# Optimization experiments

Hardware: AMD Instinct MI355X
Metric: run time of the kernel (lower is better)

The kernel has to match this reference:

```python
import jax, jax.numpy as jnp
import numpy as np

N = 50000      # nodes
E = 400000     # edges
IN = 128       # in_channels
HID = 64       # hidden_channels (per head)
H = 4          # heads
OUT = 10       # classes
G = 64         # graphs in batch


def setup_inputs() -> dict:
    key = jax.random.key(0)
    ks = jax.random.split(key, 32)
    s = 0.05
    inp = {
        "x": jax.random.normal(ks[0], (N, IN), dtype=jnp.float32),
        "edge_index": jax.random.randint(ks[1], (2, E), 0, N, dtype=jnp.int32),
        "batch": jnp.sort(jax.random.randint(ks[2], (N,), 0, G, dtype=jnp.int32)),
    }
    # TransformerConv layer 1 params (in=IN -> heads*HID)
    d1 = H * HID
    inp["Wq1"] = jax.random.normal(ks[3], (IN, d1)) * s
    inp["bq1"] = jnp.zeros((d1,), jnp.float32)
    inp["Wk1"] = jax.random.normal(ks[4], (IN, d1)) * s
    inp["bk1"] = jnp.zeros((d1,), jnp.float32)
    inp["Wv1"] = jax.random.normal(ks[5], (IN, d1)) * s
    inp["bv1"] = jnp.zeros((d1,), jnp.float32)
    inp["Ws1"] = jax.random.normal(ks[6], (IN, d1)) * s   # root/skip weight
    inp["bs1"] = jnp.zeros((d1,), jnp.float32)
    # TransformerConv layer 2 params (in=H*HID -> heads*HID)
    inp["Wq2"] = jax.random.normal(ks[7], (d1, d1)) * s
    inp["bq2"] = jnp.zeros((d1,), jnp.float32)
    inp["Wk2"] = jax.random.normal(ks[8], (d1, d1)) * s
    inp["bk2"] = jnp.zeros((d1,), jnp.float32)
    inp["Wv2"] = jax.random.normal(ks[9], (d1, d1)) * s
    inp["bv2"] = jnp.zeros((d1,), jnp.float32)
    inp["Ws2"] = jax.random.normal(ks[10], (d1, d1)) * s
    inp["bs2"] = jnp.zeros((d1,), jnp.float32)
    # final classifier
    inp["Wl"] = jax.random.normal(ks[11], (d1, OUT)) * s
    inp["bl"] = jnp.zeros((OUT,), jnp.float32)
    return inp


def transformer_conv(x, src, dst, Wq, bq, Wk, bk, Wv, bv, Ws, bs):
    """PyG TransformerConv (concat=True, root_weight=True, beta=None, eval mode).
    src = edge_index[0] (source j), dst = edge_index[1] (target i).
    """
    n = x.shape[0]
    q = (x @ Wq + bq).reshape(n, H, HID)
    k = (x @ Wk + bk).reshape(n, H, HID)
    v = (x @ Wv + bv).reshape(n, H, HID)
    # per-edge attention logits [E, H]
    alpha = jnp.einsum('ehc,ehc->eh', q[dst], k[src]) / np.sqrt(HID).astype(np.float32)
    # scatter-softmax over incoming edges of each target node
    amax = jax.ops.segment_max(alpha, dst, num_segments=n)           # [N, H], -inf for isolated
    ex = jnp.exp(alpha - amax[dst])                                   # [E, H]
    denom = jax.ops.segment_sum(ex, dst, num_segments=n) + 1e-16      # [N, H]
    w = ex / denom[dst]                                               # normalized alpha [E, H]
    # scatter-sum aggregation of weighted values
    out = jax.ops.segment_sum(w[:, :, None] * v[src], dst, num_segments=n)  # [N, H, HID]
    out = out.reshape(n, H * HID)
    return out + (x @ Ws + bs)  # root/skip connection


def reference(x, edge_index, batch,
              Wq1, bq1, Wk1, bk1, Wv1, bv1, Ws1, bs1,
              Wq2, bq2, Wk2, bk2, Wv2, bv2, Ws2, bs2,
              Wl, bl):
    src, dst = edge_index[0], edge_index[1]
    h = jax.nn.elu(transformer_conv(x, src, dst, Wq1, bq1, Wk1, bk1, Wv1, bv1, Ws1, bs1))
    h = jax.nn.elu(transformer_conv(h, src, dst, Wq2, bq2, Wk2, bk2, Wv2, bv2, Ws2, bs2))
    # global mean pool per graph
    sums = jax.ops.segment_sum(h, batch, num_segments=G)              # [G, H*HID]
    cnt = jax.ops.segment_sum(jnp.ones((h.shape[0],), h.dtype), batch, num_segments=G)
    pooled = sums / jnp.maximum(cnt, 1.0)[:, None]
    logits = pooled @ Wl + bl
    return jax.nn.log_softmax(logits, axis=-1)
```

## Files before the change

### kernel.cpp

```cpp
#include <hip/hip_runtime.h>
#include <math.h>

constexpr int NN   = 50000;
constexpr int NE   = 400000;
constexpr int INC  = 128;
constexpr int NH   = 4;
constexpr int D1   = 256;
constexpr int D4   = 1024;
constexpr int NOUT = 10;
constexpr int NG   = 64;
constexpr int NB_SCAN = (NN + 255) / 256;


typedef __attribute__((ext_vector_type(8))) short bf16x8;
typedef __attribute__((ext_vector_type(4))) float f32x4;
typedef __attribute__((ext_vector_type(2))) float f32x2;

__device__ __forceinline__ short f2b(float f) {
  union { float f; unsigned int i; } v; v.f = f;
  unsigned int x = v.i;
  return (short)((x + 0x7FFFu + ((x >> 16) & 1u)) >> 16);
}
__device__ __forceinline__ float b2f(short u) {
  union { unsigned int i; float f; } v; v.i = ((unsigned int)(unsigned short)u) << 16;
  return v.f;
}
__device__ __forceinline__ float4 ld4b(const short* p) {
  short4 u = *(const short4*)p;
  return make_float4(b2f(u.x), b2f(u.y), b2f(u.z), b2f(u.w));
}
__device__ __forceinline__ int pk_fp8x4(float a, float b, float c, float d) {
  int v = __builtin_amdgcn_cvt_pk_fp8_f32(a, b, 0, false);
  v = __builtin_amdgcn_cvt_pk_fp8_f32(c, d, v, true);
  return v;
}

__device__ __forceinline__ void gld_lds16(const short* g, short* l) {
  __builtin_amdgcn_global_load_lds(
      (const __attribute__((address_space(1))) unsigned int*)g,
      (__attribute__((address_space(3))) unsigned int*)l, 16, 0, 0);
}

constexpr int CVT_XB  = (NN * INC / 4 + 255) / 256;
constexpr int CVT_W1B = (4 * D1 * INC + 255) / 256;
constexpr int CVT_W2B = (4 * D1 * D1 + 255) / 256;
constexpr int CVT_BB  = 8;
constexpr int CVT_DB  = (NN + 255) / 256;
constexpr int CVT_SB  = (NG * D1 + 255) / 256;

__device__ __forceinline__ void wt_one(const float* Wq, const float* Wk,
    const float* Wv, const float* Ws, short* Wt, int kbits, int i) {
  int K = 1 << kbits;
  int seg = i >> (kbits + 8);
  int idx = i & ((D1 << kbits) - 1);
  int n = idx >> kbits, k = idx & (K - 1);
  const float* W = (seg == 0) ? Wq : (seg == 1) ? Wk : (seg == 2) ? Wv : Ws;
  int row;
  if (seg == 0)      row = n;
  else if (seg == 3) row = 768 + n;
  else               row = 256 + (n >> 2) * 8 + ((seg == 2) ? 4 : 0) + (n & 3);
  Wt[(size_t)row * K + k] = f2b(W[(size_t)k * D1 + n]);
}

__global__ void cvt_all_k(const float* __restrict__ x, short* __restrict__ Xb,
    const float* __restrict__ Wq1, const float* __restrict__ Wk1,
    const float* __restrict__ Wv1, const float* __restrict__ Ws1,
    const float* __restrict__ Wq2, const float* __restrict__ Wk2,
    const float* __restrict__ Wv2, const float* __restrict__ Ws2,
    short* __restrict__ Wtc1, short* __restrict__ Wtc2,
    const float* __restrict__ bq1, const float* __restrict__ bk1,
    const float* __restrict__ bv1, const float* __restrict__ bs1,
    const float* __restrict__ bq2, const float* __restrict__ bk2,
    const float* __restrict__ bv2, const float* __restrict__ bs2,
    float* __restrict__ bc1, float* __restrict__ bc2,
    int* __restrict__ deg, float* __restrict__ sums) {
  const int b = blockIdx.x;
  const int t = threadIdx.x;
  if (b < CVT_XB) {
    int i = (b * 256 + t) * 4;
    if (i >= NN * INC) return;
    float4 v = *(const float4*)(x + i);
    short4 o; o.x = f2b(v.x); o.y = f2b(v.y); o.z = f2b(v.z); o.w = f2b(v.w);
    *(short4*)(Xb + i) = o;
  } else if (b < CVT_XB + CVT_W1B) {
    int i = (b - CVT_XB) * 256 + t;
    if (i < 4 * D1 * INC) wt_one(Wq1, Wk1, Wv1, Ws1, Wtc1, 7, i);
  } else if (b < CVT_XB + CVT_W1B + CVT_W2B) {
    int i = (b - CVT_XB - CVT_W1B) * 256 + t;
    if (i < 4 * D1 * D1) wt_one(Wq2, Wk2, Wv2, Ws2, Wtc2, 8, i);
  } else if (b < CVT_XB + CVT_W1B + CVT_W2B + CVT_BB) {
    int i = (b - CVT_XB - CVT_W1B - CVT_W2B) * 256 + t;
    if (i >= 2 * D4) return;
    int row = i & (D4 - 1);
    const float* bq = (i < D4) ? bq1 : bq2;
    const float* bk = (i < D4) ? bk1 : bk2;
    const float* bv = (i < D4) ? bv1 : bv2;
    const float* bs = (i < D4) ? bs1 : bs2;
    float v;
    if (row < 256) v = bq[row];
    else if (row < 768) {
      int j = row - 256, grp = j >> 3, off = j & 7;
      int ch = grp * 4 + (off & 3);
      v = (off < 4) ? bk[ch] : bv[ch];
    } else v = bs[row - 768];
    ((i < D4) ? bc1 : bc2)[row] = v;
  } else if (b < CVT_XB + CVT_W1B + CVT_W2B + CVT_BB + CVT_DB) {
    int i = (b - CVT_XB - CVT_W1B - CVT_W2B - CVT_BB) * 256 + t;
    if (i < NN) deg[i] = 0;
  } else {
    int i = (b - CVT_XB - CVT_W1B - CVT_W2B - CVT_BB - CVT_DB) * 256 + t;
    if (i < NG * D1) sums[i] = 0.f;
  }
}

__global__ void deg_count(const int* __restrict__ dst, int* __restrict__ deg) {
  int e = blockIdx.x * 256 + threadIdx.x;
  if (e < NE) atomicAdd(&deg[dst[e]], 1);
}
__global__ __launch_bounds__(256) void scan1(const int* __restrict__ deg,
    int* __restrict__ partial, const int* __restrict__ batch, int* __restrict__ gb) {
  if (blockIdx.x == NB_SCAN) {
    int g = threadIdx.x;
    if (g > NG) return;
    int lo = 0, hi = NN;
    while (lo < hi) {
      int mid = (lo + hi) >> 1;
      if (batch[mid] < g) lo = mid + 1; else hi = mid;
    }
    gb[g] = lo;
    return;
  }
  __shared__ int sh[256];
  int t = threadIdx.x, i = blockIdx.x * 256 + t;
  sh[t] = (i < NN) ? deg[i] : 0;
  __syncthreads();
  for (int off = 128; off > 0; off >>= 1) {
    if (t < off) sh[t] += sh[t + off];
    __syncthreads();
  }
  if (t == 0) partial[blockIdx.x] = sh[0];
}
__global__ __launch_bounds__(256) void scan3(const int* __restrict__ deg,
    const int* __restrict__ partial, int* __restrict__ rowstart,
    int* __restrict__ cursor) {
  __shared__ int sh[256];
  __shared__ int base_s;
  const int t = threadIdx.x;
  int pv = (t < NB_SCAN) ? partial[t] : 0;
  sh[t] = pv;
  __syncthreads();
  for (int off = 1; off < 256; off <<= 1) {
    int o = (t >= off) ? sh[t - off] : 0;
    __syncthreads();
    sh[t] += o;
    __syncthreads();
  }
  if (t == 0) base_s = (blockIdx.x == 0) ? 0 : sh[blockIdx.x - 1];
  __syncthreads();
  const int base = base_s;
  __syncthreads();
  int i = blockIdx.x * 256 + t;
  int v = (i < NN) ? deg[i] : 0;
  sh[t] = v;
  __syncthreads();
  for (int off = 1; off < 256; off <<= 1) {
    int o = (t >= off) ? sh[t - off] : 0;
    __syncthreads();
    sh[t] += o;
    __syncthreads();
  }
  int excl = sh[t] - v + base;
  if (i <= NN) rowstart[i] = excl;
  if (i < NN)  cursor[i]   = excl;
}
__global__ void scatter_k(const int* __restrict__ src, const int* __restrict__ dst,
    int* __restrict__ cursor, int* __restrict__ esrc) {
  int e = blockIdx.x * 256 + threadIdx.x;
  if (e >= NE) return;
  int d = dst[e];
  int pos = atomicAdd(&cursor[d], 1);
  esrc[pos] = src[e];
}

constexpr int CLDS = 136;

__global__ __launch_bounds__(256) void gemm_mfma(
    const short* __restrict__ Xb, const short* __restrict__ Wt,
    const float* __restrict__ bias, short* __restrict__ QS,
    unsigned char* __restrict__ KV8, int M, int K) {
  __shared__ short smem[128 * CLDS];
  const int bx = blockIdx.x;
  const int by = blockIdx.y;
  const int m_tile = (bx & 7) + (by << 3);
  const int n_tile = bx >> 3;
  const int m0 = m_tile * 128;
  if (m0 >= M) return;
  const int n0 = n_tile * 128;

  const int t    = threadIdx.x;
  const int lane = t & 63;
  const int wv   = t >> 6;
  const int wm   = (wv >> 1) * 64;
  const int wn   = (wv & 1) * 64;
  const int quad = lane >> 4;
  const int l16  = lane & 15;
  const int lrow = lane >> 2;
  const int lseg = lane & 3;

  const int swz_w = (lseg ^ ((lrow >> 1) & 3)) * 8;
  const int swz_r = (quad ^ ((l16 >> 1) & 3)) * 8;

  f32x4 acc[4][4] = {};

  {
#pragma unroll
    for (int j = 0; j < 2; ++j) {
      const int rb = (wv * 2 + j) * 16;
      int gm = m0 + rb + lrow;
      gm = gm < M ? gm : M - 1;
      gld_lds16(Xb + (size_t)gm * K + swz_w,              &smem[rb * 32]);
      gld_lds16(Wt + (size_t)(n0 + rb + lrow) * K + swz_w, &smem[4096 + rb * 32]);
    }
  }
  __syncthreads();

  int cur = 0;
  for (int k0 = 0; k0 < K; k0 += 32) {
    if (k0 + 32 < K) {
      short* An = &smem[(cur ^ 1) * 8192];
      short* Bn = &smem[(cur ^ 1) * 8192 + 4096];
#pragma unroll
      for (int j = 0; j < 2; ++j) {
        const int rb = (wv * 2 + j) * 16;
        int gm = m0 + rb + lrow;
        gm = gm < M ? gm : M - 1;
        gld_lds16(Xb + (size_t)gm * K + k0 + 32 + swz_w,              &An[rb * 32]);
        gld_lds16(Wt + (size_t)(n0 + rb + lrow) * K + k0 + 32 + swz_w, &Bn[rb * 32]);
      }
    }
    {
      const short* Ac = &smem[cur * 8192];
      const short* Bc = &smem[cur * 8192 + 4096];
      bf16x8 a[4], b[4];
#pragma unroll
      for (int mi = 0; mi < 4; mi++)
        a[mi] = *(const bf16x8*)(&Ac[(wm + mi * 16 + l16) * 32 + swz_r]);
#pragma unroll
      for (int nj = 0; nj < 4; nj++)
        b[nj] = *(const bf16x8*)(&Bc[(wn + nj * 16 + l16) * 32 + swz_r]);
#pragma unroll
      for (int mi = 0; mi < 4; mi++)
#pragma unroll
        for (int nj = 0; nj < 4; nj++)
          acc[mi][nj] = __builtin_amdgcn_mfma_f32_16x16x32_bf16(b[nj], a[mi], acc[mi][nj], 0, 0, 0);
    }
    __syncthreads();
    cur ^= 1;
  }

  const bool isKV = (n_tile >= 2) && (n_tile <= 5);
  float4 bz[4];
#pragma unroll
  for (int nj = 0; nj < 4; nj++)
    bz[nj] = *(const float4*)(bias + n0 + wn + nj * 16 + quad * 4);

  if (isKV) {
    unsigned char* cs = (unsigned char*)smem;
#pragma unroll
    for (int mi = 0; mi < 4; mi++) {
      const int row = wm + mi * 16 + l16;
#pragma unroll
      for (int nj = 0; nj < 4; nj++) {
        const int colb = wn + nj * 16 + quad * 4;
        const int p = pk_fp8x4(acc[mi][nj][0] + bz[nj].x, acc[mi][nj][1] + bz[nj].y,
                               acc[mi][nj][2] + bz[nj].z, acc[mi][nj][3] + bz[nj].w);
        *(int*)(cs + row * 136 + colb) = p;
      }
    }
    __syncthreads();
    const int kv_base = n0 - 256;
#pragma unroll
    for (int it = 0; it < 8; ++it) {
      const int chunk = it * 256 + t;
      const int row = chunk >> 4;
      const int cb  = (chunk & 15) * 8;
      const int gm  = m0 + row;
      if (gm >= M) continue;
      *(int2*)(KV8 + (size_t)gm * 512 + kv_base + cb) = *(const int2*)(cs + row * 136 + cb);
    }
  } else {
#pragma unroll
    for (int mi = 0; mi < 4; mi++) {
      const int row = wm + mi * 16 + l16;
#pragma unroll
      for (int nj = 0; nj < 4; nj++) {
        const int col = wn + nj * 16 + quad * 4;
        short4 o;
        o.x = f2b(acc[mi][nj][0] + bz[nj].x);
        o.y = f2b(acc[mi][nj][1] + bz[nj].y);
        o.z = f2b(acc[mi][nj][2] + bz[nj].z);
        o.w = f2b(acc[mi][nj][3] + bz[nj].w);
        *(short4*)(&smem[row * CLDS + col]) = o;
      }
    }
    __syncthreads();
    const int qs_base = (n_tile < 2) ? n0 : (n0 - 512);
#pragma unroll
    for (int it = 0; it < 8; ++it) {
      const int chunk = it * 256 + t;
      const int row = chunk >> 4;
      const int cc  = (chunk & 15) * 8;
      const int gm  = m0 + row;
      if (gm >= M) continue;
      const int4 s4 = *(const int4*)(&smem[row * CLDS + cc]);
      *(int4*)(QS + (size_t)gm * 512 + qs_base + cc) = s4;
    }
  }
}

__device__ __forceinline__ f32x2 cvt_lo(int x) { return __builtin_amdgcn_cvt_pk_f32_fp8(x, false); }
__device__ __forceinline__ f32x2 cvt_hi(int x) { return __builtin_amdgcn_cvt_pk_f32_fp8(x, true); }

template <int CTRL>
__device__ __forceinline__ float ror_add(float x) {
  int y = __builtin_amdgcn_update_dpp(0, __float_as_int(x), CTRL, 0xF, 0xF, true);
  return x + __int_as_float(y);
}
__device__ __forceinline__ float red16(float x) {
  x = ror_add<0x121>(x);
  x = ror_add<0x122>(x);
  x = ror_add<0x124>(x);
  x = ror_add<0x128>(x);
  return x;
}

#define SC2 (0.125f * 1.44269504088896341f)

__device__ __forceinline__ float edge_score(const int2 x, f32x2 q01, f32x2 q23,
                                            f32x2& vv01, f32x2& vv23) {
  f32x2 kk01 = cvt_lo(x.x), kk23 = cvt_hi(x.x);
  vv01 = cvt_lo(x.y); vv23 = cvt_hi(x.y);
  f32x2 dd = q01 * kk01;
  dd += q23 * kk23;
  return red16(dd.x + dd.y);
}

template <typename TOUT>
__device__ __forceinline__ void st1(TOUT* p, float v);
template <> __device__ __forceinline__ void st1<float>(float* p, float v) { *p = v; }
template <> __device__ __forceinline__ void st1<short>(short* p, float v) { *p = f2b(v); }

template <typename TOUT>
__global__ __launch_bounds__(256) void node_attn(
    const int* __restrict__ rowstart, const int* __restrict__ esrc,
    const short* __restrict__ QS, const unsigned char* __restrict__ KV8,
    TOUT* __restrict__ out) {
  const int nid = blockIdx.x * 4 + (threadIdx.x >> 6);
  if (nid >= NN) return;
  const int t  = threadIdx.x & 63;
  const int c0 = t * 4;
  const int r0 = __builtin_amdgcn_readfirstlane(rowstart[nid]);
  const int r1 = __builtin_amdgcn_readfirstlane(rowstart[nid + 1]);
  const short4 qu = *(const short4*)(QS + (size_t)nid * 512 + c0);
  const f32x2 q01 = {b2f(qu.x), b2f(qu.y)};
  const f32x2 q23 = {b2f(qu.z), b2f(qu.w)};
  const unsigned char* kvb = KV8 + t * 8;
  float m = -INFINITY, denom = 0.f;
  f32x2 a01 = {0.f, 0.f}, a23 = {0.f, 0.f};
  int r = r0;
  for (; r + 7 < r1; r += 8) {
    const int e0 = __builtin_amdgcn_readfirstlane(esrc[r + 0]);
    const int e1 = __builtin_amdgcn_readfirstlane(esrc[r + 1]);
    const int e2 = __builtin_amdgcn_readfirstlane(esrc[r + 2]);
    const int e3 = __builtin_amdgcn_readfirstlane(esrc[r + 3]);
    const int e4 = __builtin_amdgcn_readfirstlane(esrc[r + 4]);
    const int e5 = __builtin_amdgcn_readfirstlane(esrc[r + 5]);
    const int e6 = __builtin_amdgcn_readfirstlane(esrc[r + 6]);
    const int e7 = __builtin_amdgcn_readfirstlane(esrc[r + 7]);
    const int2 x0 = *(const int2*)(kvb + (size_t)e0 * 512);
    const int2 x1 = *(const int2*)(kvb + (size_t)e1 * 512);
    const int2 x2 = *(const int2*)(kvb + (size_t)e2 * 512);
    const int2 x3 = *(const int2*)(kvb + (size_t)e3 * 512);
    const int2 x4 = *(const int2*)(kvb + (size_t)e4 * 512);
    const int2 x5 = *(const int2*)(kvb + (size_t)e5 * 512);
    const int2 x6 = *(const int2*)(kvb + (size_t)e6 * 512);
    const int2 x7 = *(const int2*)(kvb + (size_t)e7 * 512);
    f32x2 v01_0, v23_0, v01_1, v23_1, v01_2, v23_2, v01_3, v23_3;
    f32x2 v01_4, v23_4, v01_5, v23_5, v01_6, v23_6, v01_7, v23_7;
    const float s0 = edge_score(x0, q01, q23, v01_0, v23_0) * SC2;
    const float s1 = edge_score(x1, q01, q23, v01_1, v23_1) * SC2;
    const float s2 = edge_score(x2, q01, q23, v01_2, v23_2) * SC2;
    const float s3 = edge_score(x3, q01, q23, v01_3, v23_3) * SC2;
    const float s4 = edge_score(x4, q01, q23, v01_4, v23_4) * SC2;
    const float s5 = edge_score(x5, q01, q23, v01_5, v23_5) * SC2;
    const float s6 = edge_score(x6, q01, q23, v01_6, v23_6) * SC2;
    const float s7 = edge_score(x7, q01, q23, v01_7, v23_7) * SC2;
    const float t01 = fmaxf(s0, s1), t23 = fmaxf(s2, s3);
    const float t45 = fmaxf(s4, s5), t67 = fmaxf(s6, s7);
    const float nm = fmaxf(fmaxf(m, fmaxf(t01, t23)), fmaxf(t45, t67));
    const float sc  = exp2f(m - nm);
    const float ex0 = exp2f(s0 - nm);
    const float ex1 = exp2f(s1 - nm);
    const float ex2 = exp2f(s2 - nm);
    const float ex3 = exp2f(s3 - nm);
    const float ex4 = exp2f(s4 - nm);
    const float ex5 = exp2f(s5 - nm);
    const float ex6 = exp2f(s6 - nm);
    const float ex7 = exp2f(s7 - nm);
    denom = denom * sc + ((ex0 + ex1) + (ex2 + ex3)) + ((ex4 + ex5) + (ex6 + ex7));
    const f32x2 scv = {sc, sc};
    a01 = a01 * scv; a23 = a23 * scv;
    a01 += f32x2{ex0, ex0} * v01_0; a23 += f32x2{ex0, ex0} * v23_0;
    a01 += f32x2{ex1, ex1} * v01_1; a23 += f32x2{ex1, ex1} * v23_1;
    a01 += f32x2{ex2, ex2} * v01_2; a23 += f32x2{ex2, ex2} * v23_2;
    a01 += f32x2{ex3, ex3} * v01_3; a23 += f32x2{ex3, ex3} * v23_3;
    a01 += f32x2{ex4, ex4} * v01_4; a23 += f32x2{ex4, ex4} * v23_4;
    a01 += f32x2{ex5, ex5} * v01_5; a23 += f32x2{ex5, ex5} * v23_5;
    a01 += f32x2{ex6, ex6} * v01_6; a23 += f32x2{ex6, ex6} * v23_6;
    a01 += f32x2{ex7, ex7} * v01_7; a23 += f32x2{ex7, ex7} * v23_7;
    m = nm;
  }
  for (; r + 3 < r1; r += 4) {
    const int e0 = __builtin_amdgcn_readfirstlane(esrc[r + 0]);
    const int e1 = __builtin_amdgcn_readfirstlane(esrc[r + 1]);
    const int e2 = __builtin_amdgcn_readfirstlane(esrc[r + 2]);
    const int e3 = __builtin_amdgcn_readfirstlane(esrc[r + 3]);
    const int2 x0 = *(const int2*)(kvb + (size_t)e0 * 512);
    const int2 x1 = *(const int2*)(kvb + (size_t)e1 * 512);
    const int2 x2 = *(const int2*)(kvb + (size_t)e2 * 512);
    const int2 x3 = *(const int2*)(kvb + (size_t)e3 * 512);
    f32x2 v01_0, v23_0, v01_1, v23_1, v01_2, v23_2, v01_3, v23_3;
    const float s0 = edge_score(x0, q01, q23, v01_0, v23_0) * SC2;
    const float s1 = edge_score(x1, q01, q23, v01_1, v23_1) * SC2;
    const float s2 = edge_score(x2, q01, q23, v01_2, v23_2) * SC2;
    const float s3 = edge_score(x3, q01, q23, v01_3, v23_3) * SC2;
    const float nm = fmaxf(fmaxf(m, fmaxf(s0, s1)), fmaxf(s2, s3));
    const float sc  = exp2f(m - nm);
    const float ex0 = exp2f(s0 - nm);
    const float ex1 = exp2f(s1 - nm);
    const float ex2 = exp2f(s2 - nm);
    const float ex3 = exp2f(s3 - nm);
    denom = denom * sc + ex0 + ex1 + ex2 + ex3;
    const f32x2 scv = {sc, sc};
    a01 = a01 * scv; a23 = a23 * scv;
    a01 += f32x2{ex0, ex0} * v01_0; a23 += f32x2{ex0, ex0} * v23_0;
    a01 += f32x2{ex1, ex1} * v01_1; a23 += f32x2{ex1, ex1} * v23_1;
    a01 += f32x2{ex2, ex2} * v01_2; a23 += f32x2{ex2, ex2} * v23_2;
    a01 += f32x2{ex3, ex3} * v01_3; a23 += f32x2{ex3, ex3} * v23_3;
    m = nm;
  }
  for (; r < r1; r++) {
    const int e0 = __builtin_amdgcn_readfirstlane(esrc[r]);
    const int2 x0 = *(const int2*)(kvb + (size_t)e0 * 512);
    f32x2 v01_0, v23_0;
    const float s0 = edge_score(x0, q01, q23, v01_0, v23_0) * SC2;
    const float nm = fmaxf(m, s0);
    const float sc  = exp2f(m - nm);
    const float ex0 = exp2f(s0 - nm);
    denom = denom * sc + ex0;
    const f32x2 scv = {sc, sc};
    a01 = a01 * scv; a23 = a23 * scv;
    a01 += f32x2{ex0, ex0} * v01_0; a23 += f32x2{ex0, ex0} * v23_0;
    m = nm;
  }
  const float inv = 1.0f / (denom + 1e-16f);
  const float4 sk = ld4b(QS + (size_t)nid * 512 + 256 + c0);
  float o0 = a01.x * inv + sk.x;
  float o1 = a01.y * inv + sk.y;
  float o2 = a23.x * inv + sk.z;
  float o3 = a23.y * inv + sk.w;
  o0 = o0 > 0.f ? o0 : expm1f(o0);
  o1 = o1 > 0.f ? o1 : expm1f(o1);
  o2 = o2 > 0.f ? o2 : expm1f(o2);
  o3 = o3 > 0.f ? o3 : expm1f(o3);
  TOUT* p = out + (size_t)nid * D1 + c0;
  st1<TOUT>(p + 0, o0); st1<TOUT>(p + 1, o1);
  st1<TOUT>(p + 2, o2); st1<TOUT>(p + 3, o3);
}

__global__ __launch_bounds__(256) void pool_k(const float* __restrict__ h,
    const int* __restrict__ batch, float* __restrict__ sums) {
  const int c = threadIdx.x;
  const int n0 = blockIdx.x * 64;
  const int n1 = min(n0 + 64, NN);
  float run = 0.f;
  int curg = -1;
  for (int n = n0; n < n1; n++) {
    int g = batch[n];
    if (g != curg) {
      if (curg >= 0) atomicAdd(&sums[(size_t)curg * D1 + c], run);
      run = 0.f; curg = g;
    }
    run += h[(size_t)n * D1 + c];
  }
  if (curg >= 0) atomicAdd(&sums[(size_t)curg * D1 + c], run);
}

__global__ __launch_bounds__(640) void head_k(const float* __restrict__ sums,
    const int* __restrict__ gb, const float* __restrict__ Wl,
    const float* __restrict__ bl, float* __restrict__ out) {
  __shared__ float logits[NG][NOUT];
  const int t = threadIdx.x;
  if (t < NG * NOUT) {
    int g = t / NOUT, o = t % NOUT;
    float inv = 1.0f / fmaxf((float)(gb[g + 1] - gb[g]), 1.0f);
    float acc = 0.f;
    for (int k = 0; k < D1; k++) acc += sums[(size_t)g * D1 + k] * Wl[k * NOUT + o];
    logits[g][o] = acc * inv + bl[o];
  }
  __syncthreads();
  if (t < NG) {
    float mx = -INFINITY;
#pragma unroll
    for (int o = 0; o < NOUT; o++) mx = fmaxf(mx, logits[t][o]);
    float s = 0.f;
#pragma unroll
    for (int o = 0; o < NOUT; o++) s += __expf(logits[t][o] - mx);
    float lse = mx + logf(s);
#pragma unroll
    for (int o = 0; o < NOUT; o++) out[t * NOUT + o] = logits[t][o] - lse;
  }
}

extern "C" void kernel_launch(void* const* d_in, const int* in_sizes, int n_in,
                              void* d_out, int out_size, void* d_ws, size_t ws_size,
                              hipStream_t stream) {
  const float* x   = (const float*)d_in[0];
  const int* ei    = (const int*)d_in[1];
  const int* batch = (const int*)d_in[2];
  const float* Wq1 = (const float*)d_in[3];  const float* bq1 = (const float*)d_in[4];
  const float* Wk1 = (const float*)d_in[5];  const float* bk1 = (const float*)d_in[6];
  const float* Wv1 = (const float*)d_in[7];  const float* bv1 = (const float*)d_in[8];
  const float* Ws1 = (const float*)d_in[9];  const float* bs1 = (const float*)d_in[10];
  const float* Wq2 = (const float*)d_in[11]; const float* bq2 = (const float*)d_in[12];
  const float* Wk2 = (const float*)d_in[13]; const float* bk2 = (const float*)d_in[14];
  const float* Wv2 = (const float*)d_in[15]; const float* bv2 = (const float*)d_in[16];
  const float* Ws2 = (const float*)d_in[17]; const float* bs2 = (const float*)d_in[18];
  const float* Wl  = (const float*)d_in[19]; const float* bl  = (const float*)d_in[20];

  const int* srcIdx = ei;
  const int* dstIdx = ei + NE;

  float* ws = (float*)d_ws;
  const size_t SZ_NODE = (size_t)NN * D1;
  float* H2f  = ws;
  float* sums = ws + SZ_NODE;
  float* bc1  = sums + (size_t)NG * D1;
  float* bc2  = bc1 + D4;
  short* Xb   = (short*)(bc2 + D4);
  short* H1b  = Xb + (size_t)NN * INC;
  short* QS   = H1b + SZ_NODE;
  short* Wtc1 = QS + (size_t)NN * 512;
  short* Wtc2 = Wtc1 + (size_t)D4 * INC;
  unsigned char* KV8 = (unsigned char*)(Wtc2 + (size_t)D4 * D1);
  int* ip      = (int*)(KV8 + (size_t)NN * 512);
  int* deg     = ip;
  int* partial = deg + NN;
  int* rowstart= partial + 256;
  int* cursor  = rowstart + NN + 1;
  int* esrc    = cursor + NN;
  int* gb      = esrc + NE;

  const int mtiles = (NN + 127) / 128;
  const dim3 gemmGrid(64, (mtiles + 7) / 8);
  const int edgeBlocks = (NE + 255) / 256;
  const int aggBlocks  = (NN + 3) / 4;
  const int cvtBlocks  = CVT_XB + CVT_W1B + CVT_W2B + CVT_BB + CVT_DB + CVT_SB;

  cvt_all_k<<<cvtBlocks, 256, 0, stream>>>(x, Xb,
      Wq1, Wk1, Wv1, Ws1, Wq2, Wk2, Wv2, Ws2, Wtc1, Wtc2,
      bq1, bk1, bv1, bs1, bq2, bk2, bv2, bs2, bc1, bc2, deg, sums);

  deg_count<<<edgeBlocks, 256, 0, stream>>>(dstIdx, deg);
  scan1<<<NB_SCAN + 1, 256, 0, stream>>>(deg, partial, batch, gb);
  scan3<<<NB_SCAN, 256, 0, stream>>>(deg, partial, rowstart, cursor);
  scatter_k<<<edgeBlocks, 256, 0, stream>>>(srcIdx, dstIdx, cursor, esrc);

  gemm_mfma<<<gemmGrid, 256, 0, stream>>>(Xb, Wtc1, bc1, QS, KV8, NN, INC);
  node_attn<short><<<aggBlocks, 256, 0, stream>>>(rowstart, esrc, QS, KV8, H1b);

  gemm_mfma<<<gemmGrid, 256, 0, stream>>>(H1b, Wtc2, bc2, QS, KV8, NN, D1);
  node_attn<float><<<aggBlocks, 256, 0, stream>>>(rowstart, esrc, QS, KV8, H2f);

  pool_k<<<(NN + 63) / 64, 256, 0, stream>>>(H2f, batch, sums);
  head_k<<<1, 640, 0, stream>>>(sums, gb, Wl, bl, (float*)d_out);
}
```

Baseline: 357.6 us.

## Shrink GEMM epilogue LDS via two-pass staging and use packed bf16 convert

The GEMM epilogue now stages output through shared memory in two halves, one 64-row wave pair at a time. This cuts the shared buffer from 128x136 to 16384 shorts, and launch bounds now request 4 blocks per SM so more blocks can be resident. The scalar bf16 rounding is replaced by the hardware v_cvt_pk_bf16_f32 instruction. The cost is an extra barrier round in the epilogue, possible register pressure from the occupancy hint, and the smaller buffer must still hold the double-buffered main-loop tiles.

```diff
diff --git a/kernel.cpp b/kernel.cpp
--- a/kernel.cpp
+++ b/kernel.cpp
@@ -28,6 +28,11 @@
 __device__ __forceinline__ float4 ld4b(const short* p) {
   short4 u = *(const short4*)p;
   return make_float4(b2f(u.x), b2f(u.y), b2f(u.z), b2f(u.w));
+}
+__device__ __forceinline__ int cvt_pk_bf16(float lo, float hi) {
+  int r;
+  asm volatile("v_cvt_pk_bf16_f32 %0, %1, %2" : "=v"(r) : "v"(lo), "v"(hi));
+  return r;
 }
 __device__ __forceinline__ int pk_fp8x4(float a, float b, float c, float d) {
   int v = __builtin_amdgcn_cvt_pk_fp8_f32(a, b, 0, false);
@@ -184,11 +189,11 @@
 
 constexpr int CLDS = 136;
 
-__global__ __launch_bounds__(256) void gemm_mfma(
+__global__ __launch_bounds__(256, 4) void gemm_mfma(
     const short* __restrict__ Xb, const short* __restrict__ Wt,
     const float* __restrict__ bias, short* __restrict__ QS,
     unsigned char* __restrict__ KV8, int M, int K) {
-  __shared__ short smem[128 * CLDS];
+  __shared__ short smem[16384];
   const int bx = blockIdx.x;
   const int by = blockIdx.y;
   const int m_tile = (bx & 7) + (by << 3);
@@ -263,58 +268,64 @@
 #pragma unroll
   for (int nj = 0; nj < 4; nj++)
     bz[nj] = *(const float4*)(bias + n0 + wn + nj * 16 + quad * 4);
-
-  if (isKV) {
-    unsigned char* cs = (unsigned char*)smem;
-#pragma unroll
-    for (int mi = 0; mi < 4; mi++) {
-      const int row = wm + mi * 16 + l16;
-#pragma unroll
-      for (int nj = 0; nj < 4; nj++) {
-        const int colb = wn + nj * 16 + quad * 4;
-        const int p = pk_fp8x4(acc[mi][nj][0] + bz[nj].x, acc[mi][nj][1] + bz[nj].y,
-                               acc[mi][nj][2] + bz[nj].z, acc[mi][nj][3] + bz[nj].w);
-        *(int*)(cs + row * 136 + colb) = p;
+  const int kv_base = n0 - 256;
+  const int qs_base = (n_tile < 2) ? n0 : (n0 - 512);
+
+#pragma unroll
+  for (int p = 0; p < 2; ++p) {
+    if ((wv >> 1) == p) {
+      if (isKV) {
+        unsigned char* cs = (unsigned char*)smem;
+#pragma unroll
+        for (int mi = 0; mi < 4; mi++) {
+          const int row = mi * 16 + l16;
+#pragma unroll
+          for (int nj = 0; nj < 4; nj++) {
+            const int colb = wn + nj * 16 + quad * 4;
+            const int pk = pk_fp8x4(acc[mi][nj][0] + bz[nj].x, acc[mi][nj][1] + bz[nj].y,
+                                    acc[mi][nj][2] + bz[nj].z, acc[mi][nj][3] + bz[nj].w);
+            *(int*)(cs + row * 136 + colb) = pk;
+          }
+        }
+      } else {
+#pragma unroll
+        for (int mi = 0; mi < 4; mi++) {
+          const int row = mi * 16 + l16;
+#pragma unroll
+          for (int nj = 0; nj < 4; nj++) {
+            const int col = wn + nj * 16 + quad * 4;
+            int2 o;
+            o.x = cvt_pk_bf16(acc[mi][nj][0] + bz[nj].x, acc[mi][nj][1] + bz[nj].y);
+            o.y = cvt_pk_bf16(acc[mi][nj][2] + bz[nj].z, acc[mi][nj][3] + bz[nj].w);
+            *(int2*)(&smem[row * CLDS + col]) = o;
+          }
+        }
       }
     }
     __syncthreads();
-    const int kv_base = n0 - 256;
-#pragma unroll
-    for (int it = 0; it < 8; ++it) {
-      const int chunk = it * 256 + t;
-      const int row = chunk >> 4;
-      const int cb  = (chunk & 15) * 8;
-      const int gm  = m0 + row;
-      if (gm >= M) continue;
-      *(int2*)(KV8 + (size_t)gm * 512 + kv_base + cb) = *(const int2*)(cs + row * 136 + cb);
-    }
-  } else {
-#pragma unroll
-    for (int mi = 0; mi < 4; mi++) {
-      const int row = wm + mi * 16 + l16;
-#pragma unroll
-      for (int nj = 0; nj < 4; nj++) {
-        const int col = wn + nj * 16 + quad * 4;
-        short4 o;
-        o.x = f2b(acc[mi][nj][0] + bz[nj].x);
-        o.y = f2b(acc[mi][nj][1] + bz[nj].y);
-        o.z = f2b(acc[mi][nj][2] + bz[nj].z);
-        o.w = f2b(acc[mi][nj][3] + bz[nj].w);
-        *(short4*)(&smem[row * CLDS + col]) = o;
+    if (isKV) {
+      const unsigned char* cs = (const unsigned char*)smem;
+#pragma unroll
+      for (int it = 0; it < 4; ++it) {
+        const int chunk = it * 256 + t;
+        const int row = chunk >> 4;
+        const int cb  = (chunk & 15) * 8;
+        const int gm  = m0 + p * 64 + row;
+        if (gm < M)
+          *(int2*)(KV8 + (size_t)gm * 512 + kv_base + cb) = *(const int2*)(cs + row * 136 + cb);
       }
-    }
-    __syncthreads();
-    const int qs_base = (n_tile < 2) ? n0 : (n0 - 512);
-#pragma unroll
-    for (int it = 0; it < 8; ++it) {
-      const int chunk = it * 256 + t;
-      const int row = chunk >> 4;
-      const int cc  = (chunk & 15) * 8;
-      const int gm  = m0 + row;
-      if (gm >= M) continue;
-      const int4 s4 = *(const int4*)(&smem[row * CLDS + cc]);
-      *(int4*)(QS + (size_t)gm * 512 + qs_base + cc) = s4;
-    }
+    } else {
+#pragma unroll
+      for (int it = 0; it < 4; ++it) {
+        const int chunk = it * 256 + t;
+        const int row = chunk >> 4;
+        const int cc  = (chunk & 15) * 8;
+        const int gm  = m0 + p * 64 + row;
+        if (gm < M)
+          *(int4*)(QS + (size_t)gm * 512 + qs_base + cc) = *(const int4*)(&smem[row * CLDS + cc]);
+      }
+    }
+    if (p == 0) __syncthreads();
   }
 }
 
```

Measured after the change: 347.5 us. -2.8%, faster.
